# Performance work log

Hardware: AMD Instinct MI355X
Metric: run time of the kernel (lower is better)

Reference implementation:

```python
import jax, jax.numpy as jnp
import numpy as np

B, L, DIM, H = 2, 2048, 3072, 24
D = DIM // H  # head_dim = 128
EPS = 1e-6


def _rms_norm(x, scale):
    # matches torch RMSNorm: compute in fp32, eps=1e-6, scale of shape [D]
    x32 = x.astype(jnp.float32)
    rrms = jax.lax.rsqrt(jnp.mean(x32 * x32, axis=-1, keepdims=True) + EPS)
    return (x32 * rrms * scale.astype(jnp.float32)).astype(x.dtype)


def _apply_rope(t, pe):
    # t: [B,H,L,D]; pe: [B,1,L,D//2,2,2]
    t_ = t.astype(jnp.float32).reshape(B, H, L, D // 2, 1, 2)
    out = pe[..., 0] * t_[..., 0] + pe[..., 1] * t_[..., 1]  # [B,H,L,D//2,2]
    return out.reshape(B, H, L, D).astype(t.dtype)


def setup_inputs() -> dict:
    key = jax.random.key(0)
    ks = jax.random.split(key, 7)
    x = jax.random.normal(ks[0], (B, L, DIM), jnp.float32)
    pe = jax.random.normal(ks[1], (B, 1, L, D // 2, 2, 2), jnp.float32)
    qkv_w = jax.random.normal(ks[2], (3 * DIM, DIM), jnp.float32) * (DIM ** -0.5)
    proj_w = jax.random.normal(ks[3], (DIM, DIM), jnp.float32) * (DIM ** -0.5)
    proj_b = jnp.zeros((DIM,), jnp.float32)
    q_scale = jnp.ones((D,), jnp.float32)
    k_scale = jnp.ones((D,), jnp.float32)
    return {"x": x, "pe": pe, "qkv_w": qkv_w, "proj_w": proj_w,
            "proj_b": proj_b, "q_scale": q_scale, "k_scale": k_scale}


def reference(x, pe, qkv_w, proj_w, proj_b, q_scale, k_scale):
    # fused QKV projection: [B,L,3*DIM]
    qkv = jnp.einsum('bld,ed->ble', x, qkv_w)
    # 'B L (K H D) -> K B H L D'
    qkv = qkv.reshape(B, L, 3, H, D).transpose(2, 0, 3, 1, 4)
    q, k, v = qkv[0], qkv[1], qkv[2]
    # QK-RMSNorm over head_dim
    q = _rms_norm(q, q_scale)
    k = _rms_norm(k, k_scale)
    # RoPE
    q = _apply_rope(q, pe)
    k = _apply_rope(k, pe)
    # scaled dot-product attention (no mask)
    scores = jnp.einsum('bhqd,bhkd->bhqk', q, k) / jnp.sqrt(jnp.float32(D))
    attn = jax.nn.softmax(scores, axis=-1)
    o = jnp.einsum('bhqk,bhkd->bhqd', attn, v)
    # 'B H L D -> B L (H D)'
    o = o.transpose(0, 2, 1, 3).reshape(B, L, DIM)
    return o @ proj_w.T + proj_b
```

## Files before the change

### kernel.cpp

```cpp
#include <hip/hip_runtime.h>

typedef unsigned short ushort_t;
typedef unsigned short ushort8 __attribute__((ext_vector_type(8)));
typedef __bf16 bf16x8 __attribute__((ext_vector_type(8)));
typedef float f32x4 __attribute__((ext_vector_type(4)));
typedef float f32x16 __attribute__((ext_vector_type(16)));
typedef unsigned uint32x4 __attribute__((ext_vector_type(4)));

#define DEV __device__ __forceinline__

DEV ushort_t f2bf(float f) {
  unsigned u = __builtin_bit_cast(unsigned, f);
  u += 0x7FFFu + ((u >> 16) & 1u);
  return (ushort_t)(u >> 16);
}
DEV float bf2f(ushort_t u) {
  return __builtin_bit_cast(float, ((unsigned)u) << 16);
}
DEV void gload_lds16(const void* g, void* s) {
  __builtin_amdgcn_global_load_lds(
      (__attribute__((address_space(1))) void*)(size_t)g,
      (__attribute__((address_space(3))) void*)(size_t)s, 16, 0, 0);
}
DEV f32x4 mfma_bf16(ushort8 a, ushort8 b, f32x4 c) {
  return __builtin_amdgcn_mfma_f32_16x16x32_bf16(
      __builtin_bit_cast(bf16x8, a), __builtin_bit_cast(bf16x8, b), c, 0, 0, 0);
}
DEV f32x16 mfma32(ushort8 a, ushort8 b, f32x16 c) {
  return __builtin_amdgcn_mfma_f32_32x32x16_bf16(
      __builtin_bit_cast(bf16x8, a), __builtin_bit_cast(bf16x8, b), c, 0, 0, 0);
}
DEV f32x16 zero16() {
  f32x16 z;
#pragma unroll
  for (int i = 0; i < 16; ++i) z[i] = 0.f;
  return z;
}
DEV unsigned cvtpk(float lo, float hi2) {
  unsigned r;
  asm("v_cvt_pk_bf16_f32 %0, %1, %2" : "=v"(r) : "v"(lo), "v"(hi2));
  return r;
}
DEV void swap32(unsigned &x, unsigned &y) {
#if __has_builtin(__builtin_amdgcn_permlane32_swap)
  auto t = __builtin_amdgcn_permlane32_swap(x, y, false, false);
  x = (unsigned)t[0];
  y = (unsigned)t[1];
#else
  unsigned xs = (unsigned)__shfl_xor((int)x, 32, 64);
  unsigned ys = (unsigned)__shfl_xor((int)y, 32, 64);
  bool h = (threadIdx.x & 63) >= 32;
  unsigned nx = h ? ys : x;
  unsigned ny = h ? y : xs;
  x = nx; y = ny;
#endif
}
DEV void barx() {
  asm volatile("" ::: "memory");
  __builtin_amdgcn_s_barrier();
  asm volatile("" ::: "memory");
}
#define GATE_VM0 asm volatile("s_waitcnt vmcnt(0)" ::: "memory")
#define GATE_VM5 asm volatile("s_waitcnt vmcnt(5)" ::: "memory")
#define GATE_VM8 asm volatile("s_waitcnt vmcnt(8)" ::: "memory")

__global__ void cast_bf16(const float4* __restrict__ in,
                          ushort4* __restrict__ out, int n4) {
  int stride = gridDim.x * blockDim.x;
  for (int i = blockIdx.x * blockDim.x + threadIdx.x; i < n4; i += stride) {
    float4 v = in[i];
    out[i] = make_ushort4(f2bf(v.x), f2bf(v.y), f2bf(v.z), f2bf(v.w));
  }
}

template <int OUT_BF16, int ADD_BIAS>
__global__ __launch_bounds__(512, 2)
void gemmT(const ushort_t* __restrict__ A, const ushort_t* __restrict__ Bw,
           const float* __restrict__ bias, void* __restrict__ Cp,
           int M, int N, int K) {
  __shared__ ushort_t As[2][256 * 64];
  __shared__ ushort_t Bs[2][192 * 64];
  const int tid = threadIdx.x;
  const int w = tid >> 6, l = tid & 63;
  const int g = l >> 4, r = l & 15;
  const int wm = w >> 2, wn = w & 3;
  const int gx = gridDim.x;
  const int nwg = gx * gridDim.y;
  const int id = blockIdx.y * gx + blockIdx.x;
  const int swz = (id & 7) * (nwg >> 3) + (id >> 3);
  const int m0 = (swz / gx) * 256, n0 = (swz % gx) * 192;
  const int NT = K >> 6;

  int srow[4], soff[4];
#pragma unroll
  for (int i = 0; i < 4; ++i) {
    int u = i * 512 + tid;
    int row = u >> 3;
    srow[i] = row;
    soff[i] = ((u & 7) ^ (row & 7)) * 8;
  }

  auto stA = [&](int i, int t, int b) {
    gload_lds16(A + (size_t)(m0 + srow[i]) * K + t * 64 + soff[i],
                As[b] + (i * 512 + w * 64) * 8);
  };
  auto stB = [&](int i, int t, int b) {
    gload_lds16(Bw + (size_t)(n0 + srow[i]) * K + t * 64 + soff[i],
                Bs[b] + (i * 512 + w * 64) * 8);
  };
  auto rdA = [&](int b, int mi, int kk) -> ushort8 {
    int row = wm * 128 + mi * 16 + r;
    return *(const ushort8*)(As[b] + row * 64 + (((kk << 2) + g) ^ (r & 7)) * 8);
  };
  auto rdB = [&](int b, int ni, int kk) -> ushort8 {
    int col = wn * 48 + ni * 16 + r;
    return *(const ushort8*)(Bs[b] + col * 64 + (((kk << 2) + g) ^ (r & 7)) * 8);
  };

  f32x4 acc[8][3];
#pragma unroll
  for (int i = 0; i < 8; ++i)
#pragma unroll
    for (int j = 0; j < 3; ++j) acc[i][j] = f32x4{0.f, 0.f, 0.f, 0.f};

  ushort8 af[4][2], bf[3][2];

  stA(0, 0, 0); stA(2, 0, 0);
  stB(0, 0, 0); stB(1, 0, 0); stB(2, 0, 0);
  stA(1, 0, 0); stA(3, 0, 0);
  {
    int t1 = (NT > 1) ? 1 : 0;
    stA(0, t1, 1); stA(2, t1, 1);
    stB(0, t1, 1); stB(1, t1, 1); stB(2, t1, 1);
  }
  GATE_VM5;
  barx();

  for (int t = 0; t < NT; ++t) {
    const int db = t & 1;
    const int ts1 = (t + 1 < NT) ? t + 1 : NT - 1;
    const int ts2 = (t + 2 < NT) ? t + 2 : NT - 1;

#pragma unroll
    for (int mi = 0; mi < 4; ++mi)
#pragma unroll
      for (int kk = 0; kk < 2; ++kk) af[mi][kk] = rdA(db, mi, kk);
#pragma unroll
    for (int ni = 0; ni < 2; ++ni)
#pragma unroll
      for (int kk = 0; kk < 2; ++kk) bf[ni][kk] = rdB(db, ni, kk);
    stA(1, ts1, db ^ 1); stA(3, ts1, db ^ 1);
    barx();
    __builtin_amdgcn_s_setprio(1);
#pragma unroll
    for (int mi = 0; mi < 4; ++mi)
#pragma unroll
      for (int ni = 0; ni < 2; ++ni)
#pragma unroll
        for (int kk = 0; kk < 2; ++kk)
          acc[mi][ni] = mfma_bf16(af[mi][kk], bf[ni][kk], acc[mi][ni]);
    __builtin_amdgcn_s_setprio(0);
    barx();

#pragma unroll
    for (int kk = 0; kk < 2; ++kk) bf[2][kk] = rdB(db, 2, kk);
    barx();
    __builtin_amdgcn_s_setprio(1);
#pragma unroll
    for (int mi = 0; mi < 4; ++mi)
#pragma unroll
      for (int kk = 0; kk < 2; ++kk)
        acc[mi][2] = mfma_bf16(af[mi][kk], bf[2][kk], acc[mi][2]);
    __builtin_amdgcn_s_setprio(0);
    barx();

#pragma unroll
    for (int mi = 0; mi < 4; ++mi)
#pragma unroll
      for (int kk = 0; kk < 2; ++kk) af[mi][kk] = rdA(db, mi + 4, kk);
    barx();
    __builtin_amdgcn_s_setprio(1);
#pragma unroll
    for (int mi = 0; mi < 4; ++mi)
#pragma unroll
      for (int ni = 0; ni < 2; ++ni)
#pragma unroll
        for (int kk = 0; kk < 2; ++kk)
          acc[mi + 4][ni] = mfma_bf16(af[mi][kk], bf[ni][kk], acc[mi + 4][ni]);
    __builtin_amdgcn_s_setprio(0);
    barx();

    stA(0, ts2, db); stA(2, ts2, db);
    stB(0, ts2, db); stB(1, ts2, db); stB(2, ts2, db);
    __builtin_amdgcn_s_setprio(1);
#pragma unroll
    for (int mi = 0; mi < 4; ++mi)
#pragma unroll
      for (int kk = 0; kk < 2; ++kk)
        acc[mi + 4][2] = mfma_bf16(af[mi][kk], bf[2][kk], acc[mi + 4][2]);
    __builtin_amdgcn_s_setprio(0);
    GATE_VM5;
    barx();
  }

#pragma unroll
  for (int mi = 0; mi < 8; ++mi) {
#pragma unroll
    for (int ni = 0; ni < 3; ++ni) {
#pragma unroll
      for (int j = 0; j < 4; ++j) {
        int row = m0 + wm * 128 + mi * 16 + g * 4 + j;
        int col = n0 + wn * 48 + ni * 16 + r;
        float v = acc[mi][ni][j];
        if (ADD_BIAS) v += bias[col];
        if (OUT_BF16)
          ((ushort_t*)Cp)[(size_t)row * N + col] = f2bf(v);
        else
          ((float*)Cp)[(size_t)row * N + col] = v;
      }
    }
  }
}

__global__ __launch_bounds__(256)
void norm_rope(const ushort_t* __restrict__ qkv, const float* __restrict__ pe,
               const float* __restrict__ qs, const float* __restrict__ ksc,
               ushort_t* __restrict__ qb, ushort_t* __restrict__ kb,
               ushort_t* __restrict__ vtg) {
  __shared__ ushort_t Vt_lds[128 * 64];
  const int tid = threadIdx.x;
  const int w = tid >> 6, lane = tid & 63;
  const int tb = blockIdx.x, h = blockIdx.y;
  const int bl0 = tb * 64;
  const int b = bl0 >> 11, l0 = bl0 & 2047;
  const int i2 = lane * 2;

  const float sq0 = qs[i2], sq1 = qs[i2 + 1];
  const float sk0 = ksc[i2], sk1 = ksc[i2 + 1];
  const float QSC = 0.12751744f;

  for (int t = 0; t < 16; ++t) {
    const int bl = bl0 + w * 16 + t;
    const float4 p4 = *(const float4*)(pe + (size_t)bl * 256 + lane * 4);
    const size_t src = (size_t)bl * 9216 + h * 128 + i2;
    const size_t dst = ((size_t)(b * 24 + h) * 2048 + (bl & 2047)) * 128 + i2;
    {
      unsigned u = *(const unsigned*)(qkv + src);
      float x0 = bf2f((ushort_t)(u & 0xFFFFu)), x1 = bf2f((ushort_t)(u >> 16));
      float ss = x0 * x0 + x1 * x1;
#pragma unroll
      for (int mm = 32; mm; mm >>= 1) ss += __shfl_xor(ss, mm, 64);
      float rr = rsqrtf(ss * (1.f / 128.f) + 1e-6f);
      float y0 = x0 * rr * sq0, y1 = x1 * rr * sq1;
      float o0 = (p4.x * y0 + p4.y * y1) * QSC;
      float o1 = (p4.z * y0 + p4.w * y1) * QSC;
      *(unsigned*)(qb + dst) = (unsigned)f2bf(o0) | ((unsigned)f2bf(o1) << 16);
    }
    {
      unsigned u = *(const unsigned*)(qkv + src + 3072);
      float x0 = bf2f((ushort_t)(u & 0xFFFFu)), x1 = bf2f((ushort_t)(u >> 16));
      float ss = x0 * x0 + x1 * x1;
#pragma unroll
      for (int mm = 32; mm; mm >>= 1) ss += __shfl_xor(ss, mm, 64);
      float rr = rsqrtf(ss * (1.f / 128.f) + 1e-6f);
      float y0 = x0 * rr * sk0, y1 = x1 * rr * sk1;
      float o0 = p4.x * y0 + p4.y * y1;
      float o1 = p4.z * y0 + p4.w * y1;
      *(unsigned*)(kb + dst) = (unsigned)f2bf(o0) | ((unsigned)f2bf(o1) << 16);
    }
  }

  {
    const ushort_t* vsrc = qkv + (size_t)(bl0 + lane) * 9216 + 6144 + h * 128;
#pragma unroll
    for (int i = 0; i < 4; ++i) {
      int oct = w * 4 + i;
      ushort8 vv = *(const ushort8*)(vsrc + oct * 8);
#pragma unroll
      for (int j = 0; j < 8; ++j) {
        int d = oct * 8 + j;
        int ba = (d * 128 + lane * 2) ^ (j << 4);
        *(ushort_t*)((char*)Vt_lds + ba) = vv[j];
      }
    }
  }
  __syncthreads();

  {
    const int d = tid >> 1, half = tid & 1;
    ushort_t* orow = vtg + ((size_t)(b * 24 + h) * 128 + d) * 2048 + l0 + half * 32;
#pragma unroll
    for (int q = 0; q < 4; ++q) {
      int lb = d * 128 + half * 64 + q * 16;
      ushort8 vv = *(const ushort8*)((char*)Vt_lds + (lb ^ ((d & 7) << 4)));
      *(ushort8*)(orow + q * 8) = vv;
    }
  }
}

__global__ __launch_bounds__(256, 2)
void attn_fwd(const ushort_t* __restrict__ qb, const ushort_t* __restrict__ kb,
              const ushort_t* __restrict__ vt, ushort_t* __restrict__ ob) {
  __shared__ ushort_t Ks[2][64 * 128];
  __shared__ ushort_t Vts[2][128 * 64];
  const int tid = threadIdx.x;
  const int w = tid >> 6, l = tid & 63;
  const int c = l & 31, hi = l >> 5;
  const int id = blockIdx.y * 16 + blockIdx.x;
  const int swz = (id & 7) * 96 + (id >> 3);
  const int bh = swz >> 4;
  const int q0 = (swz & 15) * 128 + w * 32;

  const ushort_t* qrow = qb + ((size_t)bh * 2048 + q0 + c) * 128;
  ushort8 qf[8];
#pragma unroll
  for (int s = 0; s < 8; ++s)
    qf[s] = *(const ushort8*)(qrow + s * 16 + hi * 8);

  f32x16 o[4];
#pragma unroll
  for (int dt = 0; dt < 4; ++dt) o[dt] = zero16();
  float m = -1e30f, lp = 0.f;

  const ushort_t* kbase = kb + (size_t)bh * 2048 * 128;
  const ushort_t* vbase = vt + (size_t)bh * 128 * 2048;

  auto stage = [&](int t, int b) {
#pragma unroll
    for (int i = 0; i < 4; ++i) {
      int u = w * 256 + i * 64 + l;
      int kr = u >> 4, kc = (u & 15) ^ (kr & 15);
      gload_lds16(kbase + (size_t)(t * 64 + kr) * 128 + kc * 8,
                  Ks[b] + (w * 256 + i * 64) * 8);
      int vr = u >> 3, vc = (u & 7) ^ (vr & 7);
      gload_lds16(vbase + (size_t)vr * 2048 + t * 64 + vc * 8,
                  Vts[b] + (w * 256 + i * 64) * 8);
    }
  };

  stage(0, 0);

  for (int t = 0; t < 32; ++t) {
    const int db = t & 1;
    if (t < 31) {
      stage(t + 1, db ^ 1);
      GATE_VM8;
    } else {
      GATE_VM0;
    }
    barx();

    f32x16 s0 = zero16(), s1 = zero16();
    __builtin_amdgcn_s_setprio(1);
#pragma unroll
    for (int ds = 0; ds < 8; ++ds) {
      int ch = (2 * ds + hi) ^ (c & 15);
      ushort8 k0 = *(const ushort8*)(Ks[db] + c * 128 + ch * 8);
      ushort8 k1 = *(const ushort8*)(Ks[db] + (32 + c) * 128 + ch * 8);
      s0 = mfma32(k0, qf[ds], s0);
      s1 = mfma32(k1, qf[ds], s1);
    }
    __builtin_amdgcn_s_setprio(0);

    float p[32];
#pragma unroll
    for (int rr = 0; rr < 16; ++rr) { p[rr] = s0[rr]; p[16 + rr] = s1[rr]; }
    float pmax = p[0];
#pragma unroll
    for (int rr = 1; rr < 32; ++rr) pmax = fmaxf(pmax, p[rr]);
    if (!__all(pmax <= m + 8.f)) {
      float wm = pmax;
#pragma unroll
      for (int d = 1; d < 64; d <<= 1) wm = fmaxf(wm, __shfl_xor(wm, d, 64));
      float mn = fmaxf(m, wm);
      float fs = exp2f(m - mn);
      m = mn;
      lp *= fs;
#pragma unroll
      for (int dt = 0; dt < 4; ++dt)
#pragma unroll
        for (int e = 0; e < 16; ++e) o[dt][e] *= fs;
    }
    float rs = 0.f;
#pragma unroll
    for (int rr = 0; rr < 32; ++rr) { p[rr] = exp2f(p[rr] - m); rs += p[rr]; }
    lp += rs;

    uint32x4 pk[4];
#pragma unroll
    for (int ks = 0; ks < 4; ++ks) {
      unsigned a0 = cvtpk(p[ks * 8 + 0], p[ks * 8 + 1]);
      unsigned a1 = cvtpk(p[ks * 8 + 2], p[ks * 8 + 3]);
      unsigned a2 = cvtpk(p[ks * 8 + 4], p[ks * 8 + 5]);
      unsigned a3 = cvtpk(p[ks * 8 + 6], p[ks * 8 + 7]);
      swap32(a0, a2);
      swap32(a1, a3);
      pk[ks] = uint32x4{a0, a1, a2, a3};
    }

    __builtin_amdgcn_s_setprio(1);
#pragma unroll
    for (int dt = 0; dt < 4; ++dt) {
#pragma unroll
      for (int ks = 0; ks < 4; ++ks) {
        int ch = (2 * ks + hi) ^ (c & 7);
        ushort8 vf = *(const ushort8*)(Vts[db] + (32 * dt + c) * 64 + ch * 8);
        o[dt] = mfma32(__builtin_bit_cast(ushort8, pk[ks]), vf, o[dt]);
      }
    }
    __builtin_amdgcn_s_setprio(0);
    barx();
  }

  float lr = lp + __shfl_xor(lp, 32, 64);
  float rl = 1.f / lr;
  const int b = bh / 24, h = bh % 24;
  ushort_t* obase = ob + ((size_t)b * 2048 + q0) * 3072 + h * 128 + c;
#pragma unroll
  for (int rr = 0; rr < 16; ++rr) {
    int q = (rr & 3) + 8 * (rr >> 2) + 4 * hi;
    float os = __shfl(rl, q, 64);
#pragma unroll
    for (int dt = 0; dt < 4; ++dt)
      obase[(size_t)q * 3072 + dt * 32] = f2bf(o[dt][rr] * os);
  }
}

extern "C" void kernel_launch(void* const* d_in, const int* in_sizes, int n_in,
                              void* d_out, int out_size, void* d_ws, size_t ws_size,
                              hipStream_t stream) {
  const float* x    = (const float*)d_in[0];
  const float* pe   = (const float*)d_in[1];
  const float* qkvw = (const float*)d_in[2];
  const float* pw   = (const float*)d_in[3];
  const float* pb   = (const float*)d_in[4];
  const float* qsc  = (const float*)d_in[5];
  const float* ksc  = (const float*)d_in[6];
  float* out = (float*)d_out;

  char* p = (char*)d_ws;
  ushort_t* x_bf  = (ushort_t*)(p + 0);
  ushort_t* o_bf  = x_bf;
  ushort_t* qw_bf = (ushort_t*)(p + 25165824);
  ushort_t* pw_bf = (ushort_t*)(p + 81788928);
  ushort_t* qkv   = (ushort_t*)(p + 100663296);
  ushort_t* qh    = (ushort_t*)(p + 176160768);
  ushort_t* kh    = (ushort_t*)(p + 201326592);
  ushort_t* vtg   = (ushort_t*)(p + 226492416);

  cast_bf16<<<2048, 256, 0, stream>>>((const float4*)x,    (ushort4*)x_bf,  4096 * 3072 / 4);
  cast_bf16<<<2048, 256, 0, stream>>>((const float4*)qkvw, (ushort4*)qw_bf, 9216 * 3072 / 4);
  cast_bf16<<<2048, 256, 0, stream>>>((const float4*)pw,   (ushort4*)pw_bf, 3072 * 3072 / 4);

  gemmT<1, 0><<<dim3(48, 16), 512, 0, stream>>>(x_bf, qw_bf, nullptr, qkv, 4096, 9216, 3072);
  norm_rope<<<dim3(64, 24), 256, 0, stream>>>(qkv, pe, qsc, ksc, qh, kh, vtg);
  attn_fwd<<<dim3(16, 48), 256, 0, stream>>>(qh, kh, vtg, o_bf);
  gemmT<0, 1><<<dim3(16, 16), 512, 0, stream>>>(o_bf, pw_bf, pb, out, 4096, 3072, 3072);
}
```

Before: 522.0 us.

## Switch projection GEMM to 32x32x16 MFMA with 4x2 warp tiling and simpler prefetch

Rewrites the GEMM inner loop to use 32x32x16 bf16 MFMA instructions with a 4x2 warp layout, where each warp computes a 64x96 tile. This replaces the 16x16 MFMA path with 2x4 warps. The staged multi-barrier pipeline with two-ahead partial prefetch becomes a plain double buffer: the whole next tile is issued up front and waited on with vmcnt(0) before one barrier per K step. Larger MFMAs cut LDS reads per FLOP, but the simpler pipeline may expose more global-load latency and leave less room for overlap.

```diff
diff --git a/kernel.cpp b/kernel.cpp
--- a/kernel.cpp
+++ b/kernel.cpp
@@ -21,10 +21,6 @@
   __builtin_amdgcn_global_load_lds(
       (__attribute__((address_space(1))) void*)(size_t)g,
       (__attribute__((address_space(3))) void*)(size_t)s, 16, 0, 0);
-}
-DEV f32x4 mfma_bf16(ushort8 a, ushort8 b, f32x4 c) {
-  return __builtin_amdgcn_mfma_f32_16x16x32_bf16(
-      __builtin_bit_cast(bf16x8, a), __builtin_bit_cast(bf16x8, b), c, 0, 0, 0);
 }
 DEV f32x16 mfma32(ushort8 a, ushort8 b, f32x16 c) {
   return __builtin_amdgcn_mfma_f32_32x32x16_bf16(
@@ -61,7 +57,6 @@
   asm volatile("" ::: "memory");
 }
 #define GATE_VM0 asm volatile("s_waitcnt vmcnt(0)" ::: "memory")
-#define GATE_VM5 asm volatile("s_waitcnt vmcnt(5)" ::: "memory")
 #define GATE_VM8 asm volatile("s_waitcnt vmcnt(8)" ::: "memory")
 
 __global__ void cast_bf16(const float4* __restrict__ in,
@@ -82,8 +77,8 @@
   __shared__ ushort_t Bs[2][192 * 64];
   const int tid = threadIdx.x;
   const int w = tid >> 6, l = tid & 63;
-  const int g = l >> 4, r = l & 15;
-  const int wm = w >> 2, wn = w & 3;
+  const int c = l & 31, hi = l >> 5;
+  const int wm = w >> 1, wn = w & 1;
   const int gx = gridDim.x;
   const int nwg = gx * gridDim.y;
   const int id = blockIdx.y * gx + blockIdx.x;
@@ -108,110 +103,61 @@
     gload_lds16(Bw + (size_t)(n0 + srow[i]) * K + t * 64 + soff[i],
                 Bs[b] + (i * 512 + w * 64) * 8);
   };
-  auto rdA = [&](int b, int mi, int kk) -> ushort8 {
-    int row = wm * 128 + mi * 16 + r;
-    return *(const ushort8*)(As[b] + row * 64 + (((kk << 2) + g) ^ (r & 7)) * 8);
+  auto rdA = [&](int b, int mi, int ks) -> ushort8 {
+    int row = wm * 64 + mi * 32 + c;
+    return *(const ushort8*)(As[b] + row * 64 + ((2 * ks + hi) ^ (c & 7)) * 8);
   };
-  auto rdB = [&](int b, int ni, int kk) -> ushort8 {
-    int col = wn * 48 + ni * 16 + r;
-    return *(const ushort8*)(Bs[b] + col * 64 + (((kk << 2) + g) ^ (r & 7)) * 8);
+  auto rdB = [&](int b, int ni, int ks) -> ushort8 {
+    int row = wn * 96 + ni * 32 + c;
+    return *(const ushort8*)(Bs[b] + row * 64 + ((2 * ks + hi) ^ (c & 7)) * 8);
   };
 
-  f32x4 acc[8][3];
-#pragma unroll
-  for (int i = 0; i < 8; ++i)
-#pragma unroll
-    for (int j = 0; j < 3; ++j) acc[i][j] = f32x4{0.f, 0.f, 0.f, 0.f};
-
-  ushort8 af[4][2], bf[3][2];
-
-  stA(0, 0, 0); stA(2, 0, 0);
+  f32x16 acc[2][3];
+#pragma unroll
+  for (int i = 0; i < 2; ++i)
+#pragma unroll
+    for (int j = 0; j < 3; ++j) acc[i][j] = zero16();
+
+  stA(0, 0, 0); stA(1, 0, 0); stA(2, 0, 0); stA(3, 0, 0);
   stB(0, 0, 0); stB(1, 0, 0); stB(2, 0, 0);
-  stA(1, 0, 0); stA(3, 0, 0);
-  {
-    int t1 = (NT > 1) ? 1 : 0;
-    stA(0, t1, 1); stA(2, t1, 1);
-    stB(0, t1, 1); stB(1, t1, 1); stB(2, t1, 1);
-  }
-  GATE_VM5;
+  GATE_VM0;
   barx();
 
   for (int t = 0; t < NT; ++t) {
     const int db = t & 1;
-    const int ts1 = (t + 1 < NT) ? t + 1 : NT - 1;
-    const int ts2 = (t + 2 < NT) ? t + 2 : NT - 1;
-
-#pragma unroll
-    for (int mi = 0; mi < 4; ++mi)
-#pragma unroll
-      for (int kk = 0; kk < 2; ++kk) af[mi][kk] = rdA(db, mi, kk);
-#pragma unroll
-    for (int ni = 0; ni < 2; ++ni)
-#pragma unroll
-      for (int kk = 0; kk < 2; ++kk) bf[ni][kk] = rdB(db, ni, kk);
-    stA(1, ts1, db ^ 1); stA(3, ts1, db ^ 1);
+    const bool pre = (t + 1 < NT);
+    if (pre) {
+      stA(0, t + 1, db ^ 1); stA(1, t + 1, db ^ 1);
+      stA(2, t + 1, db ^ 1); stA(3, t + 1, db ^ 1);
+      stB(0, t + 1, db ^ 1); stB(1, t + 1, db ^ 1); stB(2, t + 1, db ^ 1);
+    }
+    asm volatile("" ::: "memory");
+    __builtin_amdgcn_s_setprio(1);
+#pragma unroll
+    for (int ks = 0; ks < 4; ++ks) {
+      ushort8 a0 = rdA(db, 0, ks), a1 = rdA(db, 1, ks);
+      ushort8 b0 = rdB(db, 0, ks), b1 = rdB(db, 1, ks), b2 = rdB(db, 2, ks);
+      acc[0][0] = mfma32(a0, b0, acc[0][0]);
+      acc[0][1] = mfma32(a0, b1, acc[0][1]);
+      acc[0][2] = mfma32(a0, b2, acc[0][2]);
+      acc[1][0] = mfma32(a1, b0, acc[1][0]);
+      acc[1][1] = mfma32(a1, b1, acc[1][1]);
+      acc[1][2] = mfma32(a1, b2, acc[1][2]);
+    }
+    __builtin_amdgcn_s_setprio(0);
+    if (pre) GATE_VM0;
     barx();
-    __builtin_amdgcn_s_setprio(1);
-#pragma unroll
-    for (int mi = 0; mi < 4; ++mi)
-#pragma unroll
-      for (int ni = 0; ni < 2; ++ni)
-#pragma unroll
-        for (int kk = 0; kk < 2; ++kk)
-          acc[mi][ni] = mfma_bf16(af[mi][kk], bf[ni][kk], acc[mi][ni]);
-    __builtin_amdgcn_s_setprio(0);
-    barx();
-
-#pragma unroll
-    for (int kk = 0; kk < 2; ++kk) bf[2][kk] = rdB(db, 2, kk);
-    barx();
-    __builtin_amdgcn_s_setprio(1);
-#pragma unroll
-    for (int mi = 0; mi < 4; ++mi)
-#pragma unroll
-      for (int kk = 0; kk < 2; ++kk)
-        acc[mi][2] = mfma_bf16(af[mi][kk], bf[2][kk], acc[mi][2]);
-    __builtin_amdgcn_s_setprio(0);
-    barx();
-
-#pragma unroll
-    for (int mi = 0; mi < 4; ++mi)
-#pragma unroll
-      for (int kk = 0; kk < 2; ++kk) af[mi][kk] = rdA(db, mi + 4, kk);
-    barx();
-    __builtin_amdgcn_s_setprio(1);
-#pragma unroll
-    for (int mi = 0; mi < 4; ++mi)
-#pragma unroll
-      for (int ni = 0; ni < 2; ++ni)
-#pragma unroll
-        for (int kk = 0; kk < 2; ++kk)
-          acc[mi + 4][ni] = mfma_bf16(af[mi][kk], bf[ni][kk], acc[mi + 4][ni]);
-    __builtin_amdgcn_s_setprio(0);
-    barx();
-
-    stA(0, ts2, db); stA(2, ts2, db);
-    stB(0, ts2, db); stB(1, ts2, db); stB(2, ts2, db);
-    __builtin_amdgcn_s_setprio(1);
-#pragma unroll
-    for (int mi = 0; mi < 4; ++mi)
-#pragma unroll
-      for (int kk = 0; kk < 2; ++kk)
-        acc[mi + 4][2] = mfma_bf16(af[mi][kk], bf[2][kk], acc[mi + 4][2]);
-    __builtin_amdgcn_s_setprio(0);
-    GATE_VM5;
-    barx();
-  }
-
-#pragma unroll
-  for (int mi = 0; mi < 8; ++mi) {
+  }
+
+#pragma unroll
+  for (int mi = 0; mi < 2; ++mi) {
 #pragma unroll
     for (int ni = 0; ni < 3; ++ni) {
 #pragma unroll
-      for (int j = 0; j < 4; ++j) {
-        int row = m0 + wm * 128 + mi * 16 + g * 4 + j;
-        int col = n0 + wn * 48 + ni * 16 + r;
-        float v = acc[mi][ni][j];
+      for (int reg = 0; reg < 16; ++reg) {
+        int row = m0 + wm * 64 + mi * 32 + (reg & 3) + 8 * (reg >> 2) + 4 * hi;
+        int col = n0 + wn * 96 + ni * 32 + c;
+        float v = acc[mi][ni][reg];
         if (ADD_BIAS) v += bias[col];
         if (OUT_BF16)
           ((ushort_t*)Cp)[(size_t)row * N + col] = f2bf(v);
```

Measured after the change: 548.1 us. 5.0% more time.
